# Optimization experiments

Hardware: AMD Instinct MI355X
Metric: run time of the kernel (lower is better)

## Reference

```python
import jax, jax.numpy as jnp
import numpy as np
import math

DIM = 1024
NH = 16
HD = DIM // NH
SEQ = 2048
B = 2
P = 16
HIDDEN = 2816  # multiple_of*ceil(int(2*4*dim/3)/multiple_of)


def justnorm(x, axis=-1):
    n = jnp.sqrt(jnp.sum(x * x, axis=axis, keepdims=True))
    return x / jnp.maximum(n, 1e-12)


def adafm_modulate(x, ftime, p):
    # x: [B,H,W]; ftime: [B, p*p] real
    Bb, H, W = x.shape
    xp = x.reshape(Bb, H // p, p, W // p, p).transpose(0, 1, 3, 2, 4).reshape(Bb, H // p, W // p, p * p)
    fspec = jnp.fft.fft2(xp)  # over last two axes (W//p, p*p)
    fspec = fspec * ftime.reshape(Bb, 1, 1, p * p)
    fout = jnp.fft.ifft2(fspec).real
    fout = fout.reshape(Bb, H // p, W // p, p, p).transpose(0, 1, 3, 2, 4).reshape(Bb, H, W)
    return fout


def apply_rotary(xq, xk, cos, sin):
    # xq,xk: [B,S,NH,HD]; cos,sin: [S, HD//2]
    def rot(t):
        tr = t.reshape(*t.shape[:-1], HD // 2, 2)
        a, b = tr[..., 0], tr[..., 1]
        c = cos[None, :, None, :]
        s = sin[None, :, None, :]
        ra = a * c - b * s
        rb = a * s + b * c
        return jnp.stack([ra, rb], axis=-1).reshape(t.shape)
    return rot(xq), rot(xk)


def attention(x, cos, sin, wq, wk, wv, wo, sqk):
    bsz, seqlen, _ = x.shape
    xq = (x @ wq).reshape(bsz, seqlen, NH, HD)
    xk = (x @ wk).reshape(bsz, seqlen, NH, HD)
    xv = (x @ wv).reshape(bsz, seqlen, NH, HD)
    xq, xk = apply_rotary(xq, xk, cos, sin)
    sqk_eff = (sqk * math.sqrt(DIM)).reshape(1, 1, NH, HD)  # sqk_init_value/sqk_init_scaling = sqrt(dim)
    xq = sqk_eff * justnorm(xq)
    xk = sqk_eff * justnorm(xk)
    scale = HD ** 0.5
    scores = jnp.einsum('bqhd,bkhd->bhqk', xq, xk) * scale
    attn = jax.nn.softmax(scores, axis=-1)
    out = jnp.einsum('bhqk,bkhd->bqhd', attn, xv).reshape(bsz, seqlen, DIM)
    return out @ wo


def feed_forward(x, w1, w2, w3, su, sv):
    x1 = x @ w1
    x3 = x @ w3
    scale = math.sqrt(HIDDEN)
    h = jax.nn.silu(x1 * sv * scale) * (x3 * su)
    return h @ w2


def setup_inputs() -> dict:
    key = jax.random.key(0)
    ks = jax.random.split(key, 12)
    inv = 1.0 / (10000.0 ** (np.arange(0, HD, 2, dtype=np.float32) / HD))
    ang = np.outer(np.arange(SEQ, dtype=np.float32), inv)
    s = 0.02
    return {
        'x': jax.random.normal(ks[0], (B, SEQ, DIM), jnp.float32),
        'freqs_cos': jnp.asarray(np.cos(ang), jnp.float32),
        'freqs_sin': jnp.asarray(np.sin(ang), jnp.float32),
        'adafm_input': jax.random.normal(ks[1], (B, DIM), jnp.float32),
        'wq': jax.random.normal(ks[2], (DIM, DIM), jnp.float32) * s,
        'wk': jax.random.normal(ks[3], (DIM, DIM), jnp.float32) * s,
        'wv': jax.random.normal(ks[4], (DIM, DIM), jnp.float32) * s,
        'wo': jax.random.normal(ks[5], (DIM, DIM), jnp.float32) * s,
        'sqk': jnp.full((DIM,), 1.0 / math.sqrt(DIM), jnp.float32),
        'w1': jax.random.normal(ks[6], (DIM, HIDDEN), jnp.float32) * s,
        'w2': jax.random.normal(ks[7], (HIDDEN, DIM), jnp.float32) * s,
        'w3': jax.random.normal(ks[8], (DIM, HIDDEN), jnp.float32) * s,
        'su': jnp.ones((HIDDEN,), jnp.float32),
        'sv': jnp.ones((HIDDEN,), jnp.float32),
        'proj_w': jax.random.normal(ks[9], (DIM, 2 * P * P), jnp.float32) * s,
        'proj_b': jnp.zeros((2 * P * P,), jnp.float32),
        'attn_alpha': jnp.full((DIM,), 0.05 / math.sqrt(DIM), jnp.float32),
        'mlp_alpha': jnp.full((DIM,), 0.05 / math.sqrt(DIM), jnp.float32),
    }


def reference(x, freqs_cos, freqs_sin, adafm_input, wq, wk, wv, wo, sqk, w1, w2, w3, su, sv, proj_w, proj_b, attn_alpha, mlp_alpha):
    # AdaFM projection: SiLU -> Linear
    t = jax.nn.silu(adafm_input) @ proj_w + proj_b  # [B, 2*P*P]
    msa_time, mlp_time = t[:, :P * P], t[:, P * P:]

    alpha_scale = 0.05 * math.sqrt(DIM)  # attn_alpha_init_value / attn_alpha_init_scaling
    lr = jnp.abs(attn_alpha * alpha_scale)
    h = justnorm(x)
    h_a = attention(adafm_modulate(x, msa_time, P), freqs_cos, freqs_sin, wq, wk, wv, wo, sqk)
    h_a = justnorm(h_a)
    x = justnorm(h + lr * (h_a - h))

    lr = jnp.abs(mlp_alpha * alpha_scale)
    h = justnorm(x)
    h_m = feed_forward(adafm_modulate(x, mlp_time, P), w1, w2, w3, su, sv)
    h_m = justnorm(h_m)
    x = justnorm(h + lr * (h_m - h))
    return x
```

## Files before the change

kernel.cpp:

```cpp
#include <hip/hip_runtime.h>
#include <hip/hip_bf16.h>
#include <math.h>

#define SEQ    2048
#define DIMN   1024
#define NHEAD  16
#define HDIM   64
#define BATCH  2
#define ROWS   4096
#define HIDDEN 2816
#define FCHUNK 2048

typedef __attribute__((ext_vector_type(8))) short short8;
typedef __attribute__((ext_vector_type(4))) float f32x4;
typedef unsigned short ushort_t;
typedef __attribute__((address_space(1))) void gas_t;
typedef __attribute__((address_space(3))) void las_t;

__device__ __forceinline__ float bfbits(ushort_t u){ return __uint_as_float(((unsigned)u) << 16); }
__device__ __forceinline__ ushort_t f2bu(float f){
  __hip_bfloat16 h = __float2bfloat16(f);
  return *reinterpret_cast<ushort_t*>(&h);
}
__device__ __forceinline__ float ldv(const float* p){ return *p; }
__device__ __forceinline__ float ldv(const ushort_t* p){ return bfbits(*p); }
__device__ __forceinline__ void stv(float* p, float v){ *p = v; }
__device__ __forceinline__ void stv(ushort_t* p, float v){ *p = f2bu(v); }
__device__ __forceinline__ void async_cp16(const ushort_t* g, ushort_t* l){
  __builtin_amdgcn_global_load_lds((gas_t*)g, (las_t*)l, 16, 0, 0);
}
__device__ __forceinline__ ushort4 ld4u(const float* p){
  float4 v = *(const float4*)p;
  ushort4 u; u.x = f2bu(v.x); u.y = f2bu(v.y); u.z = f2bu(v.z); u.w = f2bu(v.w);
  return u;
}
__device__ __forceinline__ ushort4 ld4u(const ushort_t* p){ return *(const ushort4*)p; }

__global__ void k_time(const float* __restrict__ ada, const float* __restrict__ pw,
                       const float* __restrict__ pb, float* __restrict__ t){
  int b = blockIdx.x >> 9, o = blockIdx.x & 511, lane = threadIdx.x;
  float acc = 0.f;
  for(int i = lane; i < DIMN; i += 64){
    float a = ada[b*DIMN + i];
    float s = a / (1.f + expf(-a));
    acc += s * pw[i*512 + o];
  }
  for(int off = 32; off; off >>= 1) acc += __shfl_down(acc, off);
  if(lane == 0) t[b*512 + o] = acc + pb[o];
}

__global__ void k_g(const float* __restrict__ t, float* __restrict__ g){
  int which = blockIdx.x >> 1, b = blockIdx.x & 1, n = threadIdx.x;
  const float C = 6.283185307179586f / 256.f;
  float acc = 0.f;
  for(int k = 0; k < 256; k++){
    float f = t[b*512 + which*256 + k];
    acc += f * cosf(C * (float)((k*n) & 255));
  }
  g[(which*2 + b)*256 + n] = acc * (1.f/256.f);
}

__global__ void k_gpack(const float* __restrict__ g, ushort_t* __restrict__ Gpk){
  int wb = blockIdx.x, kc = blockIdx.y, tid = threadIdx.x;
  const float* gb = g + wb*256;
  ushort_t* ob = Gpk + ((size_t)(wb*8 + kc))*8192;
  for(int rep = 0; rep < 4; rep++){
    int n = rep*64 + (tid >> 2), mmb = (tid & 3)*8;
    short8 o;
    #pragma unroll
    for(int j = 0; j < 8; j++)
      o[j] = (short)f2bu(gb[(n - kc*32 - (mmb + j)) & 255]);
    *(short8*)(ob + n*32 + mmb) = o;
  }
}

#define APAD 264
#define GPAD 40
template<typename IN>
__global__ __launch_bounds__(256) void k_modmf(const IN* __restrict__ src,
        const ushort_t* __restrict__ Gpk, ushort_t* __restrict__ dst){
  __shared__ __align__(16) ushort_t Ap[64*APAD];
  __shared__ __align__(16) ushort_t Gs[128*GPAD];
  int nh = blockIdx.x, i = blockIdx.y, b = blockIdx.z;
  int tid = threadIdx.x, lane = tid & 63, w = tid >> 6;
  int l15 = lane & 15, quad = lane >> 4;
  const IN* xb = src + (size_t)b*SEQ*DIMN + (size_t)(i*16)*DIMN;
  int j = tid >> 2, c = (tid & 3)*4;
  #pragma unroll 4
  for(int rep = 0; rep < 16; rep++){
    ushort4 v4 = ld4u(xb + (size_t)rep*DIMN + tid*4);
    *(ushort4*)&Ap[j*APAD + rep*16 + c] = v4;
  }
  f32x4 acc[8];
  #pragma unroll
  for(int nt = 0; nt < 8; nt++){ acc[nt][0]=0.f; acc[nt][1]=0.f; acc[nt][2]=0.f; acc[nt][3]=0.f; }
  for(int kc = 0; kc < 8; kc++){
    __syncthreads();
    {
      const ushort_t* gsrc = Gpk + ((size_t)(b*8 + kc))*8192 + nh*4096;
      #pragma unroll
      for(int r2 = 0; r2 < 2; r2++){
        int idx = r2*2048 + tid*8;
        int n = r2*64 + (tid >> 2), mm = (tid & 3)*8;
        *(short8*)&Gs[n*GPAD + mm] = *(const short8*)(gsrc + idx);
      }
    }
    __syncthreads();
    short8 af = *(const short8*)&Ap[(w*16 + l15)*APAD + kc*32 + quad*8];
    #pragma unroll
    for(int nt = 0; nt < 8; nt++){
      short8 bf = *(const short8*)&Gs[(nt*16 + l15)*GPAD + quad*8];
      acc[nt] = __builtin_amdgcn_mfma_f32_16x16x32_bf16(af, bf, acc[nt], 0, 0, 0);
    }
  }
  size_t ob = (size_t)b*SEQ*DIMN + (size_t)(i*16 + nh*8)*DIMN + (w*16 + quad*4)*16 + l15;
  #pragma unroll
  for(int nt = 0; nt < 8; nt++)
    #pragma unroll
    for(int t = 0; t < 4; t++)
      dst[ob + (size_t)nt*DIMN + t*16] = f2bu(acc[nt][t]);
}

__global__ void k_wt(const float* __restrict__ W, ushort_t* __restrict__ Wt, int K, int N){
  __shared__ float tile[32][33];
  int k0 = blockIdx.y*32, n0 = blockIdx.x*32;
  int r = threadIdx.x >> 3, c4 = (threadIdx.x & 7)*4;
  float4 v = *(const float4*)(W + (size_t)(k0 + r)*N + n0 + c4);
  tile[r][c4+0] = v.x; tile[r][c4+1] = v.y; tile[r][c4+2] = v.z; tile[r][c4+3] = v.w;
  __syncthreads();
  ushort4 o;
  o.x = f2bu(tile[c4+0][r]); o.y = f2bu(tile[c4+1][r]);
  o.z = f2bu(tile[c4+2][r]); o.w = f2bu(tile[c4+3][r]);
  *(ushort4*)(Wt + (size_t)(n0 + r)*K + k0 + c4) = o;
}

template<int BM, int BN, typename OUT>
__global__ __launch_bounds__(256) void k_gemm_mf(const ushort_t* __restrict__ A,
        const ushort_t* __restrict__ Wt, OUT* __restrict__ C, int N, int K){
  constexpr int MT = BM/32, NT = BN/32;
  constexpr int AI = BM/64, BI = BN/64;
  __shared__ __align__(16) ushort_t As[BM*32];
  __shared__ __align__(16) ushort_t Bs[BN*32];
  int tid = threadIdx.x, lane = tid & 63, w = tid >> 6;
  int l15 = lane & 15, quad = lane >> 4;
  int m0 = blockIdx.y*BM, n0 = blockIdx.x*BN;
  int wr = (w>>1)*(BM/2), wc = (w&1)*(BN/2);
  int srow = lane >> 2, scol = (lane & 3)*8;
  const ushort_t* ag[AI]; ushort_t* al[AI];
  const ushort_t* bg[BI]; ushort_t* bl[BI];
  #pragma unroll
  for(int i = 0; i < AI; i++){
    int rb = w*AI + i;
    ag[i] = A + (size_t)(m0 + rb*16 + srow)*K + scol;
    al[i] = As + rb*512 + lane*8;
  }
  #pragma unroll
  for(int i = 0; i < BI; i++){
    int rb = w*BI + i;
    bg[i] = Wt + (size_t)(n0 + rb*16 + srow)*K + scol;
    bl[i] = Bs + rb*512 + lane*8;
  }
  f32x4 acc[MT][NT];
  #pragma unroll
  for(int mt = 0; mt < MT; mt++)
    #pragma unroll
    for(int nt = 0; nt < NT; nt++)
      for(int t = 0; t < 4; t++) acc[mt][nt][t] = 0.f;
  for(int kk = 0; kk < K; kk += 32){
    __syncthreads();
    #pragma unroll
    for(int i = 0; i < AI; i++) async_cp16(ag[i] + kk, al[i]);
    #pragma unroll
    for(int i = 0; i < BI; i++) async_cp16(bg[i] + kk, bl[i]);
    __syncthreads();
    short8 af[MT], bf[NT];
    #pragma unroll
    for(int mt = 0; mt < MT; mt++) af[mt] = *(const short8*)&As[(wr + mt*16 + l15)*32 + quad*8];
    #pragma unroll
    for(int nt = 0; nt < NT; nt++) bf[nt] = *(const short8*)&Bs[(wc + nt*16 + l15)*32 + quad*8];
    #pragma unroll
    for(int mt = 0; mt < MT; mt++)
      #pragma unroll
      for(int nt = 0; nt < NT; nt++)
        acc[mt][nt] = __builtin_amdgcn_mfma_f32_16x16x32_bf16(af[mt], bf[nt], acc[mt][nt], 0, 0, 0);
  }
  #pragma unroll
  for(int mt = 0; mt < MT; mt++)
    #pragma unroll
    for(int nt = 0; nt < NT; nt++)
      #pragma unroll
      for(int t = 0; t < 4; t++)
        stv(C + (size_t)(m0 + wr + mt*16 + quad*4 + t)*N + n0 + wc + nt*16 + l15, acc[mt][nt][t]);
}

__global__ __launch_bounds__(256) void k_ffn12(const ushort_t* __restrict__ A,
        const ushort_t* __restrict__ W1t, const ushort_t* __restrict__ W3t,
        const float* __restrict__ su, const float* __restrict__ sv,
        ushort_t* __restrict__ H, int K){
  __shared__ __align__(16) ushort_t As[128*32];
  __shared__ __align__(16) ushort_t B1s[64*32];
  __shared__ __align__(16) ushort_t B3s[64*32];
  int tid = threadIdx.x, lane = tid & 63, w = tid >> 6;
  int l15 = lane & 15, quad = lane >> 4;
  int m0 = blockIdx.y*128, n0 = blockIdx.x*64;
  int wr = (w>>1)*64, wc = (w&1)*32;
  int srow = lane >> 2, scol = (lane & 3)*8;
  const ushort_t* ag[2]; ushort_t* al[2];
  #pragma unroll
  for(int i = 0; i < 2; i++){
    int rb = w*2 + i;
    ag[i] = A + (size_t)(m0 + rb*16 + srow)*K + scol;
    al[i] = As + rb*512 + lane*8;
  }
  const ushort_t* b1g = W1t + (size_t)(n0 + w*16 + srow)*K + scol;
  const ushort_t* b3g = W3t + (size_t)(n0 + w*16 + srow)*K + scol;
  ushort_t* b1l = B1s + w*512 + lane*8;
  ushort_t* b3l = B3s + w*512 + lane*8;
  f32x4 acc1[4][2], acc3[4][2];
  #pragma unroll
  for(int mt = 0; mt < 4; mt++)
    #pragma unroll
    for(int nt = 0; nt < 2; nt++)
      for(int t = 0; t < 4; t++){ acc1[mt][nt][t] = 0.f; acc3[mt][nt][t] = 0.f; }
  for(int kk = 0; kk < K; kk += 32){
    __syncthreads();
    async_cp16(ag[0] + kk, al[0]);
    async_cp16(ag[1] + kk, al[1]);
    async_cp16(b1g + kk, b1l);
    async_cp16(b3g + kk, b3l);
    __syncthreads();
    short8 af[4], b1f[2], b3f[2];
    #pragma unroll
    for(int mt = 0; mt < 4; mt++) af[mt] = *(const short8*)&As[(wr + mt*16 + l15)*32 + quad*8];
    #pragma unroll
    for(int nt = 0; nt < 2; nt++){
      b1f[nt] = *(const short8*)&B1s[(wc + nt*16 + l15)*32 + quad*8];
      b3f[nt] = *(const short8*)&B3s[(wc + nt*16 + l15)*32 + quad*8];
    }
    #pragma unroll
    for(int mt = 0; mt < 4; mt++)
      #pragma unroll
      for(int nt = 0; nt < 2; nt++){
        acc1[mt][nt] = __builtin_amdgcn_mfma_f32_16x16x32_bf16(af[mt], b1f[nt], acc1[mt][nt], 0, 0, 0);
        acc3[mt][nt] = __builtin_amdgcn_mfma_f32_16x16x32_bf16(af[mt], b3f[nt], acc3[mt][nt], 0, 0, 0);
      }
  }
  #pragma unroll
  for(int nt = 0; nt < 2; nt++){
    int n = n0 + wc + nt*16 + l15;
    float svv = sv[n] * 53.06599665f, suv = su[n];
    #pragma unroll
    for(int mt = 0; mt < 4; mt++)
      #pragma unroll
      for(int t = 0; t < 4; t++){
        float hpre = acc1[mt][nt][t] * svv;
        float sil = hpre / (1.f + expf(-hpre));
        float hv = sil * (acc3[mt][nt][t] * suv);
        H[(size_t)(m0 + wr + mt*16 + quad*4 + t)*HIDDEN + n] = f2bu(hv);
      }
  }
}

__global__ void k_qkvprep(ushort_t* __restrict__ xq, ushort_t* __restrict__ xk,
        const float* __restrict__ fc, const float* __restrict__ fs,
        const float* __restrict__ sqk){
  int w = threadIdx.x >> 6, d = threadIdx.x & 63;
  int h = blockIdx.x*4 + w, s = blockIdx.y, b = blockIdx.z;
  size_t ib = ((size_t)(b*SEQ + s))*DIMN + h*HDIM + d;
  float q = bfbits(xq[ib]), k = bfbits(xk[ib]);
  float qn = __shfl_xor(q, 1), kn = __shfl_xor(k, 1);
  int p = d >> 1;
  float c = fc[s*32 + p], sn = fs[s*32 + p];
  float qr, kr;
  if((d & 1) == 0){ qr = q*c - qn*sn; kr = k*c - kn*sn; }
  else            { qr = qn*sn + q*c; kr = kn*sn + k*c; }
  float sq = qr*qr, sk = kr*kr;
  for(int off = 32; off; off >>= 1){ sq += __shfl_xor(sq, off); sk += __shfl_xor(sk, off); }
  float scl = sqk[h*HDIM + d] * 32.f;
  xq[ib] = f2bu(scl * qr / fmaxf(sqrtf(sq), 1e-12f));
  xk[ib] = f2bu(scl * kr / fmaxf(sqrtf(sk), 1e-12f));
}

__global__ void k_vt(const ushort_t* __restrict__ v, ushort_t* __restrict__ vto){
  __shared__ ushort_t tile[64][72];
  int s0 = blockIdx.x*64, h = blockIdx.y, b = blockIdx.z;
  int r = threadIdx.x >> 2, c = (threadIdx.x & 3)*16;
  const ushort_t* src = v + (size_t)(b*SEQ + s0 + r)*DIMN + h*HDIM + c;
  *(short8*)&tile[r][c]     = *(const short8*)src;
  *(short8*)&tile[r][c + 8] = *(const short8*)(src + 8);
  __syncthreads();
  ushort_t* dst = vto + ((size_t)(b*NHEAD + h)*HDIM + r)*SEQ + s0 + c;
  for(int j = 0; j < 16; j += 4){
    ushort4 o;
    o.x = tile[c+j][r]; o.y = tile[c+j+1][r]; o.z = tile[c+j+2][r]; o.w = tile[c+j+3][r];
    *(ushort4*)(dst + j) = o;
  }
}

#define LSTR 72
__global__ __launch_bounds__(256) void k_flash_mf(const ushort_t* __restrict__ qp,
        const ushort_t* __restrict__ kp, const ushort_t* __restrict__ vt,
        ushort_t* __restrict__ out){
  int qb = blockIdx.x, h = blockIdx.y, b = blockIdx.z;
  int tid = threadIdx.x, lane = tid & 63, w = tid >> 6;
  int l15 = lane & 15, quad = lane >> 4;
  __shared__ __align__(16) ushort_t Ks[64*LSTR], Vts[64*LSTR];
  __shared__ __align__(16) ushort_t Ps[4][16*LSTR];
  size_t hb = (size_t)b*SEQ*DIMN + h*HDIM;
  const ushort_t* vb = vt + (size_t)(b*NHEAD + h)*HDIM*SEQ;
  short8 qf0, qf1;
  {
    const ushort_t* qrow = qp + hb + (size_t)(qb*64 + w*16 + l15)*DIMN;
    qf0 = *(const short8*)(qrow + quad*8);
    qf1 = *(const short8*)(qrow + 32 + quad*8);
  }
  f32x4 o_acc[4];
  #pragma unroll
  for(int g = 0; g < 4; g++) for(int t = 0; t < 4; t++) o_acc[g][t] = 0.f;
  float lsum = 0.f;
  int sr = tid >> 2, sc = tid & 3;
  const float C1 = 11.54156036f;
  const float C2 = 11.90223409f;
  for(int ch = 0; ch < SEQ/64; ch++){
    __syncthreads();
    {
      const ushort_t* krow = kp + hb + (size_t)(ch*64 + sr)*DIMN + sc*16;
      short8 k0 = *(const short8*)krow, k1 = *(const short8*)(krow + 8);
      const ushort_t* vrow = vb + (size_t)sr*SEQ + ch*64 + sc*16;
      short8 v0 = *(const short8*)vrow, v1 = *(const short8*)(vrow + 8);
      *(short8*)&Ks[sr*LSTR + sc*16]      = k0;
      *(short8*)&Ks[sr*LSTR + sc*16 + 8]  = k1;
      *(short8*)&Vts[sr*LSTR + sc*16]     = v0;
      *(short8*)&Vts[sr*LSTR + sc*16 + 8] = v1;
    }
    __syncthreads();
    #pragma unroll
    for(int g = 0; g < 4; g++){
      f32x4 sa; sa[0] = 0.f; sa[1] = 0.f; sa[2] = 0.f; sa[3] = 0.f;
      short8 k0 = *(const short8*)&Ks[(g*16 + l15)*LSTR + quad*8];
      short8 k1 = *(const short8*)&Ks[(g*16 + l15)*LSTR + 32 + quad*8];
      sa = __builtin_amdgcn_mfma_f32_16x16x32_bf16(k0, qf0, sa, 0, 0, 0);
      sa = __builtin_amdgcn_mfma_f32_16x16x32_bf16(k1, qf1, sa, 0, 0, 0);
      float e0 = exp2f(fmaf(sa[0], C1, -C2));
      float e1 = exp2f(fmaf(sa[1], C1, -C2));
      float e2 = exp2f(fmaf(sa[2], C1, -C2));
      float e3 = exp2f(fmaf(sa[3], C1, -C2));
      lsum += (e0 + e1) + (e2 + e3);
      ushort4 pk;
      pk.x = f2bu(e0); pk.y = f2bu(e1); pk.z = f2bu(e2); pk.w = f2bu(e3);
      *(ushort4*)&Ps[w][l15*LSTR + g*16 + quad*4] = pk;
    }
    short8 a0 = *(const short8*)&Ps[w][l15*LSTR + quad*8];
    short8 a1 = *(const short8*)&Ps[w][l15*LSTR + 32 + quad*8];
    #pragma unroll
    for(int g = 0; g < 4; g++){
      short8 b0 = *(const short8*)&Vts[(g*16 + l15)*LSTR + quad*8];
      short8 b1 = *(const short8*)&Vts[(g*16 + l15)*LSTR + 32 + quad*8];
      o_acc[g] = __builtin_amdgcn_mfma_f32_16x16x32_bf16(a0, b0, o_acc[g], 0, 0, 0);
      o_acc[g] = __builtin_amdgcn_mfma_f32_16x16x32_bf16(a1, b1, o_acc[g], 0, 0, 0);
    }
  }
  lsum += __shfl_xor(lsum, 16);
  lsum += __shfl_xor(lsum, 32);
  #pragma unroll
  for(int t = 0; t < 4; t++){
    float lr = __shfl(lsum, quad*4 + t);
    float inv = 1.f / lr;
    #pragma unroll
    for(int g = 0; g < 4; g++)
      out[hb + (size_t)(qb*64 + w*16 + quad*4 + t)*DIMN + g*16 + l15] = f2bu(o_acc[g][t] * inv);
  }
}

__device__ __forceinline__ float blockReduceSum(float v, float* red){
  for(int off = 32; off; off >>= 1) v += __shfl_xor(v, off);
  int wid = threadIdx.x >> 6;
  if((threadIdx.x & 63) == 0) red[wid] = v;
  __syncthreads();
  float tot = red[0] + red[1] + red[2] + red[3];
  __syncthreads();
  return tot;
}

template<typename T1, typename T2, typename TO>
__global__ void k_rn(const T1* __restrict__ x, const T2* __restrict__ ha,
        const float* __restrict__ alpha, TO* __restrict__ xo){
  __shared__ float red[4];
  int row = blockIdx.x, tid = threadIdx.x;
  size_t base = (size_t)row * DIMN;
  float xs[4], hs[4], cs[4];
  float s1 = 0.f, s2 = 0.f;
  for(int j = 0; j < 4; j++){
    int i = tid + j*256;
    float xv = ldv(x + base + i);  xs[j] = xv; s1 += xv*xv;
    float hv = ldv(ha + base + i); hs[j] = hv; s2 += hv*hv;
  }
  s1 = blockReduceSum(s1, red);
  s2 = blockReduceSum(s2, red);
  float r1 = 1.f / fmaxf(sqrtf(s1), 1e-12f);
  float r2 = 1.f / fmaxf(sqrtf(s2), 1e-12f);
  float s3 = 0.f;
  for(int j = 0; j < 4; j++){
    int i = tid + j*256;
    float lr = fabsf(alpha[i] * 1.6f);
    float hn = xs[j] * r1;
    float cv = hn + lr*(hs[j]*r2 - hn);
    cs[j] = cv; s3 += cv*cv;
  }
  s3 = blockReduceSum(s3, red);
  float r3 = 1.f / fmaxf(sqrtf(s3), 1e-12f);
  for(int j = 0; j < 4; j++){
    int i = tid + j*256;
    stv(xo + base + i, cs[j] * r3);
  }
}

extern "C" void kernel_launch(void* const* d_in, const int* in_sizes, int n_in,
                              void* d_out, int out_size, void* d_ws, size_t ws_size,
                              hipStream_t stream){
  const float* x   = (const float*)d_in[0];
  const float* fc  = (const float*)d_in[1];
  const float* fs  = (const float*)d_in[2];
  const float* ada = (const float*)d_in[3];
  const float* wq  = (const float*)d_in[4];
  const float* wk  = (const float*)d_in[5];
  const float* wv  = (const float*)d_in[6];
  const float* wo  = (const float*)d_in[7];
  const float* sqk = (const float*)d_in[8];
  const float* w1  = (const float*)d_in[9];
  const float* w2  = (const float*)d_in[10];
  const float* w3  = (const float*)d_in[11];
  const float* su  = (const float*)d_in[12];
  const float* sv  = (const float*)d_in[13];
  const float* pw  = (const float*)d_in[14];
  const float* pb  = (const float*)d_in[15];
  const float* aal = (const float*)d_in[16];
  const float* mal = (const float*)d_in[17];
  float* out = (float*)d_out;

  const size_t MM = (size_t)DIMN*DIMN;
  const size_t HM = (size_t)HIDDEN*DIMN;
  const size_t F  = (size_t)ROWS*DIMN;
  char* wsb = (char*)d_ws;
  float* t = (float*)wsb;
  float* g = t + 1024;
  ushort_t* Gpk = (ushort_t*)(wsb + 16384);
  ushort_t* wqT = Gpk + 262144;
  ushort_t* wkT = wqT + MM;
  ushort_t* wvT = wkT + MM;
  ushort_t* woT = wvT + MM;
  ushort_t* w1T = woT + MM;
  ushort_t* w3T = w1T + HM;
  ushort_t* w2T = w3T + HM;
  ushort_t* P1  = w2T + HM;
  ushort_t* P2  = P1 + F;
  ushort_t* Kb  = P2 + F;
  ushort_t* Vb  = Kb + F;
  ushort_t* a1  = Vb + F;
  ushort_t* Vt  = a1;

  dim3 blk(256);

  k_time<<<dim3(1024), dim3(64), 0, stream>>>(ada, pw, pb, t);
  k_g<<<dim3(4), blk, 0, stream>>>(t, g);
  k_gpack<<<dim3(4,8), blk, 0, stream>>>(g, Gpk);

  k_wt<<<dim3(32,32), blk, 0, stream>>>(wq, wqT, DIMN, DIMN);
  k_wt<<<dim3(32,32), blk, 0, stream>>>(wk, wkT, DIMN, DIMN);
  k_wt<<<dim3(32,32), blk, 0, stream>>>(wv, wvT, DIMN, DIMN);
  k_wt<<<dim3(32,32), blk, 0, stream>>>(wo, woT, DIMN, DIMN);
  k_wt<<<dim3(HIDDEN/32,32), blk, 0, stream>>>(w1, w1T, DIMN, HIDDEN);
  k_wt<<<dim3(HIDDEN/32,32), blk, 0, stream>>>(w3, w3T, DIMN, HIDDEN);
  k_wt<<<dim3(32,HIDDEN/32), blk, 0, stream>>>(w2, w2T, HIDDEN, DIMN);

  k_modmf<float><<<dim3(2,128,BATCH), blk, 0, stream>>>(x, Gpk, P1);
  k_gemm_mf<128,64,ushort_t><<<dim3(16,32), blk, 0, stream>>>(P1, wqT, P2, DIMN, DIMN);
  k_gemm_mf<128,64,ushort_t><<<dim3(16,32), blk, 0, stream>>>(P1, wkT, Kb, DIMN, DIMN);
  k_gemm_mf<128,64,ushort_t><<<dim3(16,32), blk, 0, stream>>>(P1, wvT, Vb, DIMN, DIMN);
  k_qkvprep<<<dim3(NHEAD/4,SEQ,BATCH), blk, 0, stream>>>(P2, Kb, fc, fs, sqk);
  k_vt<<<dim3(SEQ/64,NHEAD,BATCH), blk, 0, stream>>>(Vb, Vt);
  k_flash_mf<<<dim3(SEQ/64,NHEAD,BATCH), blk, 0, stream>>>(P2, Kb, Vt, P1);
  k_gemm_mf<128,64,ushort_t><<<dim3(16,32), blk, 0, stream>>>(P1, woT, Vb, DIMN, DIMN);
  k_rn<float,ushort_t,ushort_t><<<dim3(ROWS), blk, 0, stream>>>(x, Vb, aal, P2);

  k_modmf<ushort_t><<<dim3(2,128,BATCH), blk, 0, stream>>>(P2, Gpk + 131072, P1);
  for(int c2 = 0; c2 < ROWS/FCHUNK; c2++){
    const ushort_t* Ac = P1 + (size_t)c2*FCHUNK*DIMN;
    k_ffn12<<<dim3(HIDDEN/64,FCHUNK/128), blk, 0, stream>>>(Ac, w1T, w3T, su, sv, a1, DIMN);
    k_gemm_mf<64,64,ushort_t><<<dim3(16,FCHUNK/64), blk, 0, stream>>>(a1, w2T, Kb + (size_t)c2*FCHUNK*DIMN, DIMN, HIDDEN);
  }

  k_rn<ushort_t,ushort_t,float><<<dim3(ROWS), blk, 0, stream>>>(P2, Kb, mal, out);
}
```

Baseline: 547.9 us.

## Fuse QKV projections into one GEMM and widen flash-attention query tiles

Replaces the three separate Q/K/V GEMMs with a single GEMM over the contiguous transposed weights, producing an interleaved [rows, 3072] QKV buffer. The rotary/norm, V-transpose and flash kernels now read from that buffer. Flash attention processes 128 query rows per block (two 16-row tiles per wave), so each loaded K/V tile is reused twice as often. Other changes: the remaining GEMMs use 128x128 tiles, the two small gain-table kernels are merged into one, and P is converted to bf16 by truncation instead of rounding. The costs are fewer blocks for occupancy, more registers in the flash kernel, an extra barrier per chunk, and slightly different P rounding.

```diff
diff --git a/kernel.cpp b/kernel.cpp
--- a/kernel.cpp
+++ b/kernel.cpp
@@ -10,6 +10,7 @@
 #define ROWS   4096
 #define HIDDEN 2816
 #define FCHUNK 2048
+#define QKVS   3072
 
 typedef __attribute__((ext_vector_type(8))) short short8;
 typedef __attribute__((ext_vector_type(4))) float f32x4;
@@ -22,6 +23,7 @@
   __hip_bfloat16 h = __float2bfloat16(f);
   return *reinterpret_cast<ushort_t*>(&h);
 }
+__device__ __forceinline__ ushort_t f2bu_t(float f){ return (ushort_t)(__float_as_uint(f) >> 16); }
 __device__ __forceinline__ float ldv(const float* p){ return *p; }
 __device__ __forceinline__ float ldv(const ushort_t* p){ return bfbits(*p); }
 __device__ __forceinline__ void stv(float* p, float v){ *p = v; }
@@ -49,27 +51,25 @@
   if(lane == 0) t[b*512 + o] = acc + pb[o];
 }
 
-__global__ void k_g(const float* __restrict__ t, float* __restrict__ g){
-  int which = blockIdx.x >> 1, b = blockIdx.x & 1, n = threadIdx.x;
+__global__ void k_gp(const float* __restrict__ t, ushort_t* __restrict__ Gpk){
+  __shared__ float gl[256];
+  int wb = blockIdx.x, kc = blockIdx.y, tid = threadIdx.x;
+  int b = wb & 1, which = wb >> 1;
   const float C = 6.283185307179586f / 256.f;
   float acc = 0.f;
   for(int k = 0; k < 256; k++){
     float f = t[b*512 + which*256 + k];
-    acc += f * cosf(C * (float)((k*n) & 255));
-  }
-  g[(which*2 + b)*256 + n] = acc * (1.f/256.f);
-}
-
-__global__ void k_gpack(const float* __restrict__ g, ushort_t* __restrict__ Gpk){
-  int wb = blockIdx.x, kc = blockIdx.y, tid = threadIdx.x;
-  const float* gb = g + wb*256;
+    acc += f * cosf(C * (float)((k*tid) & 255));
+  }
+  gl[tid] = acc * (1.f/256.f);
+  __syncthreads();
   ushort_t* ob = Gpk + ((size_t)(wb*8 + kc))*8192;
   for(int rep = 0; rep < 4; rep++){
     int n = rep*64 + (tid >> 2), mmb = (tid & 3)*8;
     short8 o;
     #pragma unroll
     for(int j = 0; j < 8; j++)
-      o[j] = (short)f2bu(gb[(n - kc*32 - (mmb + j)) & 255]);
+      o[j] = (short)f2bu(gl[(n - kc*32 - (mmb + j)) & 255]);
     *(short8*)(ob + n*32 + mmb) = o;
   }
 }
@@ -100,9 +100,8 @@
       const ushort_t* gsrc = Gpk + ((size_t)(b*8 + kc))*8192 + nh*4096;
       #pragma unroll
       for(int r2 = 0; r2 < 2; r2++){
-        int idx = r2*2048 + tid*8;
         int n = r2*64 + (tid >> 2), mm = (tid & 3)*8;
-        *(short8*)&Gs[n*GPAD + mm] = *(const short8*)(gsrc + idx);
+        *(short8*)&Gs[n*GPAD + mm] = *(const short8*)(gsrc + r2*2048 + tid*8);
       }
     }
     __syncthreads();
@@ -261,13 +260,12 @@
   }
 }
 
-__global__ void k_qkvprep(ushort_t* __restrict__ xq, ushort_t* __restrict__ xk,
-        const float* __restrict__ fc, const float* __restrict__ fs,
-        const float* __restrict__ sqk){
+__global__ void k_qkvprep(ushort_t* __restrict__ qkv, const float* __restrict__ fc,
+        const float* __restrict__ fs, const float* __restrict__ sqk){
   int w = threadIdx.x >> 6, d = threadIdx.x & 63;
   int h = blockIdx.x*4 + w, s = blockIdx.y, b = blockIdx.z;
-  size_t ib = ((size_t)(b*SEQ + s))*DIMN + h*HDIM + d;
-  float q = bfbits(xq[ib]), k = bfbits(xk[ib]);
+  size_t ib = ((size_t)(b*SEQ + s))*QKVS + h*HDIM + d;
+  float q = bfbits(qkv[ib]), k = bfbits(qkv[ib + 1024]);
   float qn = __shfl_xor(q, 1), kn = __shfl_xor(k, 1);
   int p = d >> 1;
   float c = fc[s*32 + p], sn = fs[s*32 + p];
@@ -277,15 +275,15 @@
   float sq = qr*qr, sk = kr*kr;
   for(int off = 32; off; off >>= 1){ sq += __shfl_xor(sq, off); sk += __shfl_xor(sk, off); }
   float scl = sqk[h*HDIM + d] * 32.f;
-  xq[ib] = f2bu(scl * qr / fmaxf(sqrtf(sq), 1e-12f));
-  xk[ib] = f2bu(scl * kr / fmaxf(sqrtf(sk), 1e-12f));
-}
-
-__global__ void k_vt(const ushort_t* __restrict__ v, ushort_t* __restrict__ vto){
+  qkv[ib]        = f2bu(scl * qr / fmaxf(sqrtf(sq), 1e-12f));
+  qkv[ib + 1024] = f2bu(scl * kr / fmaxf(sqrtf(sk), 1e-12f));
+}
+
+__global__ void k_vt(const ushort_t* __restrict__ qkv, ushort_t* __restrict__ vto){
   __shared__ ushort_t tile[64][72];
   int s0 = blockIdx.x*64, h = blockIdx.y, b = blockIdx.z;
   int r = threadIdx.x >> 2, c = (threadIdx.x & 3)*16;
-  const ushort_t* src = v + (size_t)(b*SEQ + s0 + r)*DIMN + h*HDIM + c;
+  const ushort_t* src = qkv + (size_t)(b*SEQ + s0 + r)*QKVS + 2048 + h*HDIM + c;
   *(short8*)&tile[r][c]     = *(const short8*)src;
   *(short8*)&tile[r][c + 8] = *(const short8*)(src + 8);
   __syncthreads();
@@ -298,33 +296,35 @@
 }
 
 #define LSTR 72
-__global__ __launch_bounds__(256) void k_flash_mf(const ushort_t* __restrict__ qp,
-        const ushort_t* __restrict__ kp, const ushort_t* __restrict__ vt,
-        ushort_t* __restrict__ out){
+__global__ __launch_bounds__(256) void k_flash_mf(const ushort_t* __restrict__ qkv,
+        const ushort_t* __restrict__ vt, ushort_t* __restrict__ out){
   int qb = blockIdx.x, h = blockIdx.y, b = blockIdx.z;
   int tid = threadIdx.x, lane = tid & 63, w = tid >> 6;
   int l15 = lane & 15, quad = lane >> 4;
   __shared__ __align__(16) ushort_t Ks[64*LSTR], Vts[64*LSTR];
-  __shared__ __align__(16) ushort_t Ps[4][16*LSTR];
-  size_t hb = (size_t)b*SEQ*DIMN + h*HDIM;
+  __shared__ __align__(16) ushort_t Ps[4][32*LSTR];
+  size_t qkb = (size_t)b*SEQ*QKVS + h*HDIM;
   const ushort_t* vb = vt + (size_t)(b*NHEAD + h)*HDIM*SEQ;
-  short8 qf0, qf1;
-  {
-    const ushort_t* qrow = qp + hb + (size_t)(qb*64 + w*16 + l15)*DIMN;
-    qf0 = *(const short8*)(qrow + quad*8);
-    qf1 = *(const short8*)(qrow + 32 + quad*8);
-  }
-  f32x4 o_acc[4];
-  #pragma unroll
-  for(int g = 0; g < 4; g++) for(int t = 0; t < 4; t++) o_acc[g][t] = 0.f;
-  float lsum = 0.f;
+  short8 qf[2][2];
+  #pragma unroll
+  for(int qm = 0; qm < 2; qm++){
+    const ushort_t* qrow = qkv + qkb + (size_t)(qb*128 + w*32 + qm*16 + l15)*QKVS;
+    qf[qm][0] = *(const short8*)(qrow + quad*8);
+    qf[qm][1] = *(const short8*)(qrow + 32 + quad*8);
+  }
+  f32x4 o_acc[2][4];
+  #pragma unroll
+  for(int qm = 0; qm < 2; qm++)
+    #pragma unroll
+    for(int g = 0; g < 4; g++){ o_acc[qm][g][0]=0.f; o_acc[qm][g][1]=0.f; o_acc[qm][g][2]=0.f; o_acc[qm][g][3]=0.f; }
+  float lsum[2] = {0.f, 0.f};
   int sr = tid >> 2, sc = tid & 3;
   const float C1 = 11.54156036f;
   const float C2 = 11.90223409f;
   for(int ch = 0; ch < SEQ/64; ch++){
     __syncthreads();
     {
-      const ushort_t* krow = kp + hb + (size_t)(ch*64 + sr)*DIMN + sc*16;
+      const ushort_t* krow = qkv + qkb + (size_t)(b ? 0 : 0) + (size_t)(ch*64 + sr)*QKVS + 1024 + sc*16;
       short8 k0 = *(const short8*)krow, k1 = *(const short8*)(krow + 8);
       const ushort_t* vrow = vb + (size_t)sr*SEQ + ch*64 + sc*16;
       short8 v0 = *(const short8*)vrow, v1 = *(const short8*)(vrow + 8);
@@ -336,39 +336,54 @@
     __syncthreads();
     #pragma unroll
     for(int g = 0; g < 4; g++){
-      f32x4 sa; sa[0] = 0.f; sa[1] = 0.f; sa[2] = 0.f; sa[3] = 0.f;
       short8 k0 = *(const short8*)&Ks[(g*16 + l15)*LSTR + quad*8];
       short8 k1 = *(const short8*)&Ks[(g*16 + l15)*LSTR + 32 + quad*8];
-      sa = __builtin_amdgcn_mfma_f32_16x16x32_bf16(k0, qf0, sa, 0, 0, 0);
-      sa = __builtin_amdgcn_mfma_f32_16x16x32_bf16(k1, qf1, sa, 0, 0, 0);
-      float e0 = exp2f(fmaf(sa[0], C1, -C2));
-      float e1 = exp2f(fmaf(sa[1], C1, -C2));
-      float e2 = exp2f(fmaf(sa[2], C1, -C2));
-      float e3 = exp2f(fmaf(sa[3], C1, -C2));
-      lsum += (e0 + e1) + (e2 + e3);
-      ushort4 pk;
-      pk.x = f2bu(e0); pk.y = f2bu(e1); pk.z = f2bu(e2); pk.w = f2bu(e3);
-      *(ushort4*)&Ps[w][l15*LSTR + g*16 + quad*4] = pk;
-    }
-    short8 a0 = *(const short8*)&Ps[w][l15*LSTR + quad*8];
-    short8 a1 = *(const short8*)&Ps[w][l15*LSTR + 32 + quad*8];
+      #pragma unroll
+      for(int qm = 0; qm < 2; qm++){
+        f32x4 sa; sa[0]=0.f; sa[1]=0.f; sa[2]=0.f; sa[3]=0.f;
+        sa = __builtin_amdgcn_mfma_f32_16x16x32_bf16(k0, qf[qm][0], sa, 0, 0, 0);
+        sa = __builtin_amdgcn_mfma_f32_16x16x32_bf16(k1, qf[qm][1], sa, 0, 0, 0);
+        float e0 = exp2f(fmaf(sa[0], C1, -C2));
+        float e1 = exp2f(fmaf(sa[1], C1, -C2));
+        float e2 = exp2f(fmaf(sa[2], C1, -C2));
+        float e3 = exp2f(fmaf(sa[3], C1, -C2));
+        lsum[qm] += (e0 + e1) + (e2 + e3);
+        ushort4 pk;
+        pk.x = f2bu_t(e0); pk.y = f2bu_t(e1); pk.z = f2bu_t(e2); pk.w = f2bu_t(e3);
+        *(ushort4*)&Ps[w][(qm*16 + l15)*LSTR + g*16 + quad*4] = pk;
+      }
+    }
+    __syncthreads();
+    short8 a[2][2];
+    #pragma unroll
+    for(int qm = 0; qm < 2; qm++){
+      a[qm][0] = *(const short8*)&Ps[w][(qm*16 + l15)*LSTR + quad*8];
+      a[qm][1] = *(const short8*)&Ps[w][(qm*16 + l15)*LSTR + 32 + quad*8];
+    }
     #pragma unroll
     for(int g = 0; g < 4; g++){
       short8 b0 = *(const short8*)&Vts[(g*16 + l15)*LSTR + quad*8];
       short8 b1 = *(const short8*)&Vts[(g*16 + l15)*LSTR + 32 + quad*8];
-      o_acc[g] = __builtin_amdgcn_mfma_f32_16x16x32_bf16(a0, b0, o_acc[g], 0, 0, 0);
-      o_acc[g] = __builtin_amdgcn_mfma_f32_16x16x32_bf16(a1, b1, o_acc[g], 0, 0, 0);
-    }
-  }
-  lsum += __shfl_xor(lsum, 16);
-  lsum += __shfl_xor(lsum, 32);
-  #pragma unroll
-  for(int t = 0; t < 4; t++){
-    float lr = __shfl(lsum, quad*4 + t);
-    float inv = 1.f / lr;
-    #pragma unroll
-    for(int g = 0; g < 4; g++)
-      out[hb + (size_t)(qb*64 + w*16 + quad*4 + t)*DIMN + g*16 + l15] = f2bu(o_acc[g][t] * inv);
+      #pragma unroll
+      for(int qm = 0; qm < 2; qm++){
+        o_acc[qm][g] = __builtin_amdgcn_mfma_f32_16x16x32_bf16(a[qm][0], b0, o_acc[qm][g], 0, 0, 0);
+        o_acc[qm][g] = __builtin_amdgcn_mfma_f32_16x16x32_bf16(a[qm][1], b1, o_acc[qm][g], 0, 0, 0);
+      }
+    }
+  }
+  #pragma unroll
+  for(int qm = 0; qm < 2; qm++){
+    float ls = lsum[qm];
+    ls += __shfl_xor(ls, 16);
+    ls += __shfl_xor(ls, 32);
+    #pragma unroll
+    for(int t = 0; t < 4; t++){
+      float inv = 1.f / __shfl(ls, quad*4 + t);
+      #pragma unroll
+      for(int g = 0; g < 4; g++)
+        out[(size_t)b*SEQ*DIMN + (size_t)(qb*128 + w*32 + qm*16 + quad*4 + t)*DIMN + h*HDIM + g*16 + l15]
+          = f2bu(o_acc[qm][g][t] * inv);
+    }
   }
 }
 
@@ -443,7 +458,6 @@
   const size_t F  = (size_t)ROWS*DIMN;
   char* wsb = (char*)d_ws;
   float* t = (float*)wsb;
-  float* g = t + 1024;
   ushort_t* Gpk = (ushort_t*)(wsb + 16384);
   ushort_t* wqT = Gpk + 262144;
   ushort_t* wkT = wqT + MM;
@@ -453,17 +467,17 @@
   ushort_t* w3T = w1T + HM;
   ushort_t* w2T = w3T + HM;
   ushort_t* P1  = w2T + HM;
-  ushort_t* P2  = P1 + F;
-  ushort_t* Kb  = P2 + F;
-  ushort_t* Vb  = Kb + F;
-  ushort_t* a1  = Vb + F;
+  ushort_t* QKV = P1 + F;
+  ushort_t* Ha  = QKV;
+  ushort_t* M2  = QKV + F;
+  ushort_t* Hm  = QKV + 2*F;
+  ushort_t* a1  = QKV + 3*F;
   ushort_t* Vt  = a1;
 
   dim3 blk(256);
 
   k_time<<<dim3(1024), dim3(64), 0, stream>>>(ada, pw, pb, t);
-  k_g<<<dim3(4), blk, 0, stream>>>(t, g);
-  k_gpack<<<dim3(4,8), blk, 0, stream>>>(g, Gpk);
+  k_gp<<<dim3(4,8), blk, 0, stream>>>(t, Gpk);
 
   k_wt<<<dim3(32,32), blk, 0, stream>>>(wq, wqT, DIMN, DIMN);
   k_wt<<<dim3(32,32), blk, 0, stream>>>(wk, wkT, DIMN, DIMN);
@@ -474,21 +488,19 @@
   k_wt<<<dim3(32,HIDDEN/32), blk, 0, stream>>>(w2, w2T, HIDDEN, DIMN);
 
   k_modmf<float><<<dim3(2,128,BATCH), blk, 0, stream>>>(x, Gpk, P1);
-  k_gemm_mf<128,64,ushort_t><<<dim3(16,32), blk, 0, stream>>>(P1, wqT, P2, DIMN, DIMN);
-  k_gemm_mf<128,64,ushort_t><<<dim3(16,32), blk, 0, stream>>>(P1, wkT, Kb, DIMN, DIMN);
-  k_gemm_mf<128,64,ushort_t><<<dim3(16,32), blk, 0, stream>>>(P1, wvT, Vb, DIMN, DIMN);
-  k_qkvprep<<<dim3(NHEAD/4,SEQ,BATCH), blk, 0, stream>>>(P2, Kb, fc, fs, sqk);
-  k_vt<<<dim3(SEQ/64,NHEAD,BATCH), blk, 0, stream>>>(Vb, Vt);
-  k_flash_mf<<<dim3(SEQ/64,NHEAD,BATCH), blk, 0, stream>>>(P2, Kb, Vt, P1);
-  k_gemm_mf<128,64,ushort_t><<<dim3(16,32), blk, 0, stream>>>(P1, woT, Vb, DIMN, DIMN);
-  k_rn<float,ushort_t,ushort_t><<<dim3(ROWS), blk, 0, stream>>>(x, Vb, aal, P2);
-
-  k_modmf<ushort_t><<<dim3(2,128,BATCH), blk, 0, stream>>>(P2, Gpk + 131072, P1);
+  k_gemm_mf<128,128,ushort_t><<<dim3(24,32), blk, 0, stream>>>(P1, wqT, QKV, QKVS, DIMN);
+  k_qkvprep<<<dim3(NHEAD/4,SEQ,BATCH), blk, 0, stream>>>(QKV, fc, fs, sqk);
+  k_vt<<<dim3(SEQ/64,NHEAD,BATCH), blk, 0, stream>>>(QKV, Vt);
+  k_flash_mf<<<dim3(SEQ/128,NHEAD,BATCH), blk, 0, stream>>>(QKV, Vt, P1);
+  k_gemm_mf<128,128,ushort_t><<<dim3(8,32), blk, 0, stream>>>(P1, woT, Ha, DIMN, DIMN);
+  k_rn<float,ushort_t,ushort_t><<<dim3(ROWS), blk, 0, stream>>>(x, Ha, aal, P1);
+
+  k_modmf<ushort_t><<<dim3(2,128,BATCH), blk, 0, stream>>>(P1, Gpk + 131072, M2);
   for(int c2 = 0; c2 < ROWS/FCHUNK; c2++){
-    const ushort_t* Ac = P1 + (size_t)c2*FCHUNK*DIMN;
+    const ushort_t* Ac = M2 + (size_t)c2*FCHUNK*DIMN;
     k_ffn12<<<dim3(HIDDEN/64,FCHUNK/128), blk, 0, stream>>>(Ac, w1T, w3T, su, sv, a1, DIMN);
-    k_gemm_mf<64,64,ushort_t><<<dim3(16,FCHUNK/64), blk, 0, stream>>>(a1, w2T, Kb + (size_t)c2*FCHUNK*DIMN, DIMN, HIDDEN);
-  }
-
-  k_rn<ushort_t,ushort_t,float><<<dim3(ROWS), blk, 0, stream>>>(P2, Kb, mal, out);
-}
+    k_gemm_mf<128,128,ushort_t><<<dim3(8,FCHUNK/128), blk, 0, stream>>>(a1, w2T, Hm + (size_t)c2*FCHUNK*DIMN, DIMN, HIDDEN);
+  }
+
+  k_rn<ushort_t,ushort_t,float><<<dim3(ROWS), blk, 0, stream>>>(P1, Hm, mal, out);
+}
```

Measured after the change: 578.5 us. 1.06x slower.
